# Kernel tuning notes

Measured on AMD Instinct MI355X. Metric: run time of the kernel, lower is better.

## Reference

```python
import jax, jax.numpy as jnp
import numpy as np

WIN_H, WIN_W = 4, 7
WIN = WIN_H * WIN_W  # 28 sample points == feature channels
GRID_OFF = (0.0, 40.0)
SPATIAL_SCALE = 1.0 / 0.4
BN_EPS = 1e-3


def setup_inputs() -> dict:
    key = jax.random.key(0)
    ks = jax.random.split(key, 5)
    B, Cin, H, W = 4, 256, 200, 176
    Cout, N = WIN, 2048
    x = jax.random.normal(ks[0], (B, Cin, H, W), dtype=jnp.float32)
    # boxes [x, y, z, w, l, h, r] in realistic KITTI ranges
    lo = jnp.array([0.0, -40.0, -3.0, 1.5, 3.2, 1.4, -np.pi], jnp.float32)
    hi = jnp.array([70.0, 40.0, 1.0, 2.0, 4.2, 1.8, np.pi], jnp.float32)
    u = jax.random.uniform(ks[1], (B, N, 7), dtype=jnp.float32)
    guided_anchors = lo + u * (hi - lo)
    w1 = jax.random.normal(ks[2], (Cout, Cin, 3, 3), jnp.float32) * 0.02
    gamma = jnp.ones((Cout,), jnp.float32)
    beta = jnp.zeros((Cout,), jnp.float32)
    running_mean = jnp.zeros((Cout,), jnp.float32)
    running_var = jnp.ones((Cout,), jnp.float32)
    w2 = jax.random.normal(ks[3], (Cout, Cout, 1, 1), jnp.float32) * 0.05
    return dict(x=x, guided_anchors=guided_anchors, w1=w1, gamma=gamma,
                beta=beta, running_mean=running_mean, running_var=running_var, w2=w2)


def _convs(x, w1, gamma, beta, mean, var, w2):
    dn = ('NCHW', 'OIHW', 'NCHW')
    y = jax.lax.conv_general_dilated(x, w1, (1, 1), 'SAME', dimension_numbers=dn)
    scale = gamma * jax.lax.rsqrt(var + BN_EPS)
    y = y * scale[:, None, None] + (beta - mean * scale)[:, None, None]  # BN (inference)
    y = jax.nn.relu(y)
    return jax.lax.conv_general_dilated(y, w2, (1, 1), 'SAME', dimension_numbers=dn)


def _gen_sample_grid(box5):
    xg, yg, wg, lg, rg = (box5[:, i] for i in range(5))
    c = jnp.cos(rg)[:, None, None]
    s = jnp.sin(rg)[:, None, None]
    xx = (jnp.linspace(-0.5, 0.5, WIN_H)[None, :] * wg[:, None])[:, :, None]  # (N,4,1)
    yy = (jnp.linspace(-0.5, 0.5, WIN_W)[None, :] * lg[:, None])[:, None, :]  # (N,1,7)
    xpix = xx * c + yy * s + xg[:, None, None]  # (N,4,7)
    ypix = yy * c - xx * s + yg[:, None, None]  # (N,4,7)
    xs = ((jnp.transpose(xpix, (1, 2, 0)) + GRID_OFF[0]) * SPATIAL_SCALE).reshape(WIN, -1)
    ys = ((jnp.transpose(ypix, (1, 2, 0)) + GRID_OFF[1]) * SPATIAL_SCALE).reshape(WIN, -1)
    return xs, ys


def _bilinear_sample(img, xs, ys):
    # img: (C,H,W); xs, ys: (C,N) pixel coords (align_corners=True semantics,
    # zero padding outside) -> (C,N). Channel c samples at grid row c.
    C, H, W = img.shape
    x0 = jnp.floor(xs); y0 = jnp.floor(ys)
    wx = xs - x0; wy = ys - y0
    cidx = jnp.arange(C)[:, None]

    def gather(yf, xf):
        yi = yf.astype(jnp.int32); xi = xf.astype(jnp.int32)
        valid = (yf >= 0) & (yf <= H - 1) & (xf >= 0) & (xf <= W - 1)
        v = img[cidx, jnp.clip(yi, 0, H - 1), jnp.clip(xi, 0, W - 1)]
        return jnp.where(valid, v, 0.0)

    return (gather(y0, x0) * (1 - wx) * (1 - wy)
            + gather(y0, x0 + 1) * wx * (1 - wy)
            + gather(y0 + 1, x0) * (1 - wx) * wy
            + gather(y0 + 1, x0 + 1) * wx * wy)


def reference(x, guided_anchors, w1, gamma, beta, running_mean, running_var, w2):
    feat = _convs(x, w1, gamma, beta, running_mean, running_var, w2)  # (B,28,H,W)
    box5 = guided_anchors[:, :, jnp.array([0, 1, 3, 4, 6])]           # (B,N,5)
    xs, ys = jax.vmap(_gen_sample_grid)(box5)                          # (B,28,N) each
    vals = jax.vmap(_bilinear_sample)(feat, xs, ys)                    # (B,28,N)
    scores = jnp.mean(vals, axis=1)                                    # (B,N)
    return scores.reshape(-1)                                          # (B*N,)
```

## Files before the change

kernel.cpp:

```cpp
#include <hip/hip_runtime.h>
#include <hip/hip_bf16.h>

#define HH 200
#define WW 176
#define CIN 256
#define CO 28
#define BN_EPS 1e-3f

typedef __attribute__((ext_vector_type(8))) short short8;
typedef __attribute__((ext_vector_type(4))) float f32x4;

static __device__ __forceinline__ ushort f2bf(float f) {
    __hip_bfloat16 h = __float2bfloat16(f);
    return __builtin_bit_cast(ushort, h);
}

__global__ void prep_k(const float* __restrict__ w1, const float* __restrict__ gamma,
                       const float* __restrict__ beta, const float* __restrict__ mean,
                       const float* __restrict__ var, ushort* __restrict__ w1b,
                       float* __restrict__ shift)
{
    int idx = blockIdx.x * 256 + threadIdx.x;
    if (idx < CO) {
        float sc = gamma[idx] * rsqrtf(var[idx] + BN_EPS);
        shift[idx] = beta[idx] - mean[idx] * sc;
    }
    if (idx < 8 * 9 * 2 * 64 * 8) {
        int j   = idx & 7;
        int l   = (idx >> 3) & 63;
        int n   = (idx >> 9) & 1;
        int rem = idx >> 10;
        int t   = rem % 9;
        int h   = rem / 9;
        int co = n * 16 + (l & 15);
        int ci = h * 32 + (l >> 4) * 8 + j;
        float v = 0.f;
        if (co < CO) {
            float sc = gamma[co] * rsqrtf(var[co] + BN_EPS);
            v = w1[(co * CIN + ci) * 9 + t] * sc;
        }
        w1b[idx] = f2bf(v);
    }
}

__global__ __launch_bounds__(256, 3) void conv_mfma_k(
    const float* __restrict__ x, const ushort* __restrict__ w1b,
    const float* __restrict__ shift, float* __restrict__ y1)
{
    __shared__ uint4 sbuf[2][180 * 4];

    const int tid  = threadIdx.x;
    const int lane = tid & 63;
    const int w    = tid >> 6;

    const int NB = 11 * 25 * 4;
    const int q = NB / 8, r = NB % 8;
    const int bid  = blockIdx.x;
    const int xcd  = bid & 7;
    const int rank = bid >> 3;
    const int tile = (xcd < r ? xcd * (q + 1) : r * (q + 1) + (xcd - r) * q) + rank;

    const int tx  = tile % 11;
    const int rem = tile / 11;
    const int ty  = rem % 25;
    const int b   = rem / 25;
    const int x0  = tx * 16, y0 = ty * 8;

    const float* xb = x + (size_t)b * CIN * HH * WW;

    int  soff[3]; bool sval[3]; bool sp[3];
#pragma unroll
    for (int it = 0; it < 3; ++it) {
        int p = it * 64 + lane;
        sp[it] = p < 180;
        int rr = p / 18, cc = p - rr * 18;
        int gy = y0 + rr - 1, gx = x0 + cc - 1;
        bool v = (gy >= 0) & (gy < HH) & (gx >= 0) & (gx < WW) & sp[it];
        sval[it] = v;
        soff[it] = v ? gy * WW + gx : 0;
    }

    float pre[3][8];

    auto issue_x = [&](int h) {
        const float* pl = xb + (size_t)(h * 32 + w * 8) * (HH * WW);
#pragma unroll
        for (int it = 0; it < 3; ++it) {
            if (sp[it]) {
#pragma unroll
                for (int j = 0; j < 8; ++j)
                    pre[it][j] = pl[(size_t)j * (HH * WW) + soff[it]];
            }
        }
    };

    auto wr_x = [&](int bi) {
#pragma unroll
        for (int it = 0; it < 3; ++it) {
            if (sp[it]) {
                int p = it * 64 + lane;
                ushort u[8];
#pragma unroll
                for (int j = 0; j < 8; ++j)
                    u[j] = sval[it] ? f2bf(pre[it][j]) : (ushort)0;
                uint4 val;
                val.x = (uint)u[0] | ((uint)u[1] << 16);
                val.y = (uint)u[2] | ((uint)u[3] << 16);
                val.z = (uint)u[4] | ((uint)u[5] << 16);
                val.w = (uint)u[6] | ((uint)u[7] << 16);
                sbuf[bi][p * 4 + ((w + p) & 3)] = val;
            }
        }
    };

    f32x4 acc[2][2];
#pragma unroll
    for (int m = 0; m < 2; ++m)
#pragma unroll
        for (int n = 0; n < 2; ++n)
            acc[m][n] = (f32x4){0.f, 0.f, 0.f, 0.f};

    issue_x(0);
    wr_x(0);
    __syncthreads();

#pragma unroll 1
    for (int h = 0; h < 8; ++h) {
        short8 wreg[9][2];
        {
            const ushort* wsrc = w1b + (size_t)h * 9216;
#pragma unroll
            for (int t = 0; t < 9; ++t)
#pragma unroll
                for (int n = 0; n < 2; ++n)
                    wreg[t][n] = *(const short8*)(wsrc + (size_t)((t * 2 + n) * 64 + lane) * 8);
        }
        if (h < 7) issue_x(h + 1);
        __builtin_amdgcn_sched_barrier(0);

        {
            const uint4* sb = sbuf[h & 1];
            short8 av[4][3];
#pragma unroll
            for (int rr = 0; rr < 4; ++rr) {
#pragma unroll
                for (int dx = 0; dx < 3; ++dx) {
                    int p = (2 * w + rr) * 18 + (lane & 15) + dx;
                    av[rr][dx] = __builtin_bit_cast(short8, sb[p * 4 + (((lane >> 4) + p) & 3)]);
                }
            }
#pragma unroll
            for (int t = 0; t < 9; ++t) {
                const int dy = t / 3, dx = t % 3;
#pragma unroll
                for (int m = 0; m < 2; ++m) {
                    short8 af = av[m + dy][dx];
                    acc[m][0] = __builtin_amdgcn_mfma_f32_16x16x32_bf16(af, wreg[t][0], acc[m][0], 0, 0, 0);
                    acc[m][1] = __builtin_amdgcn_mfma_f32_16x16x32_bf16(af, wreg[t][1], acc[m][1], 0, 0, 0);
                }
            }
        }
        __builtin_amdgcn_sched_barrier(0);

        if (h < 7) {
            wr_x((h + 1) & 1);
            __syncthreads();
        }
    }

    const int co0 = lane & 15;
    const int co1 = 16 + co0;
    const float s0 = shift[co0];
    const float s1 = (co1 < CO) ? shift[co1] : 0.f;
#pragma unroll
    for (int m = 0; m < 2; ++m) {
        int gy = y0 + 2 * w + m;
#pragma unroll
        for (int reg = 0; reg < 4; ++reg) {
            int gx = x0 + (lane >> 4) * 4 + reg;
            float* yp = y1 + ((size_t)(b * HH + gy) * WW + gx) * CO;
            float v0 = acc[m][0][reg] + s0;
            yp[co0] = v0 > 0.f ? v0 : 0.f;
            if (co1 < CO) {
                float v1 = acc[m][1][reg] + s1;
                yp[co1] = v1 > 0.f ? v1 : 0.f;
            }
        }
    }
}

__global__ __launch_bounds__(224) void sample_k(
    const float* __restrict__ y1, const float* __restrict__ ga,
    const float* __restrict__ w2, float* __restrict__ out)
{
    __shared__ float red[224];
    const int lb  = threadIdx.x / CO;
    const int k   = threadIdx.x % CO;
    const int box = blockIdx.x * 8 + lb;
    const int b   = box >> 11;

    const float* ap = ga + (size_t)box * 7;
    float xg = ap[0], yg = ap[1], wg = ap[3], lg = ap[4], rg = ap[6];
    float c = cosf(rg), s = sinf(rg);

    const int i = k / 7, j = k % 7;
    float xx = ((float)i * (1.f / 3.f) - 0.5f) * wg;
    float yy = ((float)j * (1.f / 6.f) - 0.5f) * lg;
    float xs = (xx * c + yy * s + xg) * 2.5f;
    float ys = (yy * c - xx * s + yg + 40.f) * 2.5f;

    float x0 = floorf(xs), y0 = floorf(ys);
    float wx = xs - x0,    wy = ys - y0;

    float w2r[CO];
    const float* w2p = w2 + k * CO;
#pragma unroll
    for (int q = 0; q < 7; ++q) {
        float4 t = ((const float4*)w2p)[q];
        w2r[4*q] = t.x; w2r[4*q+1] = t.y; w2r[4*q+2] = t.z; w2r[4*q+3] = t.w;
    }

    float val = 0.f;
    const float* yb = y1 + (size_t)b * HH * WW * CO;
#pragma unroll
    for (int cor = 0; cor < 4; ++cor) {
        float yf = y0 + (float)(cor >> 1);
        float xf = x0 + (float)(cor & 1);
        float cw = ((cor & 1) ? wx : 1.f - wx) * ((cor >> 1) ? wy : 1.f - wy);
        if (yf >= 0.f && yf <= (float)(HH - 1) && xf >= 0.f && xf <= (float)(WW - 1)) {
            int yi = (int)yf, xi = (int)xf;
            const float* p = yb + ((size_t)yi * WW + xi) * CO;
            float d = 0.f;
#pragma unroll
            for (int q = 0; q < 7; ++q) {
                float4 t = ((const float4*)p)[q];
                d = fmaf(w2r[4*q],   t.x, d);
                d = fmaf(w2r[4*q+1], t.y, d);
                d = fmaf(w2r[4*q+2], t.z, d);
                d = fmaf(w2r[4*q+3], t.w, d);
            }
            val = fmaf(cw, d, val);
        }
    }

    red[threadIdx.x] = val;
    __syncthreads();
    if (k == 0) {
        float sum = 0.f;
#pragma unroll
        for (int q = 0; q < CO; ++q) sum += red[lb * CO + q];
        out[box] = sum * (1.f / 28.f);
    }
}

extern "C" void kernel_launch(void* const* d_in, const int* in_sizes, int n_in,
                              void* d_out, int out_size, void* d_ws, size_t ws_size,
                              hipStream_t stream) {
    const float* x     = (const float*)d_in[0];
    const float* ga    = (const float*)d_in[1];
    const float* w1    = (const float*)d_in[2];
    const float* gamma = (const float*)d_in[3];
    const float* beta  = (const float*)d_in[4];
    const float* mean  = (const float*)d_in[5];
    const float* var   = (const float*)d_in[6];
    const float* w2    = (const float*)d_in[7];
    float* out = (float*)d_out;

    ushort* w1b   = (ushort*)d_ws;
    float*  shift = (float*)((char*)d_ws + 147456);
    float*  y1    = (float*)((char*)d_ws + 147968);

    prep_k<<<(8 * 9 * 2 * 64 * 8 + 255) / 256, 256, 0, stream>>>(
        w1, gamma, beta, mean, var, w1b, shift);

    conv_mfma_k<<<11 * 25 * 4, 256, 0, stream>>>(x, w1b, shift, y1);

    sample_k<<<(4 * 2048) / 8, 224, 0, stream>>>(y1, ga, w2, out);
}
```

Baseline: 86.49 us.

## Pre-transpose input to padded NHWC bf16 and drop LDS staging in conv

Adds two kernels: one zeroes the borders of a padded buffer, the other converts the NCHW fp32 input into a spatially padded NHWC bf16 layout. The conv kernel then reads A fragments straight from global memory as 16-byte vectors, with no LDS double-buffering, no barriers and no per-iteration bounds checks, and loads weights per tap instead of holding them all in registers. Occupancy is raised to 4 waves per SIMD. The cost is an extra full pass that reads x and writes a roughly 74 MB intermediate, and the conv now relies on cache for the 3x3 reuse rather than on LDS.

```diff
diff --git a/kernel.cpp b/kernel.cpp
--- a/kernel.cpp
+++ b/kernel.cpp
@@ -5,6 +5,8 @@
 #define WW 176
 #define CIN 256
 #define CO 28
+#define XH 202
+#define XW 178
 #define BN_EPS 1e-3f
 
 typedef __attribute__((ext_vector_type(8))) short short8;
@@ -43,12 +45,61 @@
     }
 }
 
-__global__ __launch_bounds__(256, 3) void conv_mfma_k(
-    const float* __restrict__ x, const ushort* __restrict__ w1b,
+__global__ __launch_bounds__(256) void pad_k(ushort* __restrict__ xtp)
+{
+    const int row = blockIdx.x;
+    const int y   = row % XH;
+    uint4* base = (uint4*)(xtp + (size_t)row * XW * 256);
+    const uint4 z = {0u, 0u, 0u, 0u};
+    if (y == 0 || y == XH - 1) {
+        for (int i = threadIdx.x; i < XW * 32; i += 256) base[i] = z;
+    } else if (threadIdx.x < 64) {
+        int px = threadIdx.x >> 5;
+        int i  = threadIdx.x & 31;
+        base[(px ? (XW - 1) : 0) * 32 + i] = z;
+    }
+}
+
+__global__ __launch_bounds__(256) void xt_k(const float* __restrict__ x,
+                                            ushort* __restrict__ xtp)
+{
+    const int bid = blockIdx.x;
+    const int xc  = bid % 11;
+    const int rem = bid / 11;
+    const int y   = rem % HH;
+    const int b   = rem / HH;
+    const int px  = threadIdx.x & 15;
+    const int cig = threadIdx.x >> 4;
+    const int gx  = xc * 16 + px;
+
+    const float* xp = x + ((size_t)b * CIN + cig * 16) * (HH * WW) + y * WW + gx;
+    float v[16];
+#pragma unroll
+    for (int j = 0; j < 16; ++j) v[j] = xp[(size_t)j * (HH * WW)];
+
+    ushort u[16];
+#pragma unroll
+    for (int j = 0; j < 16; ++j) u[j] = f2bf(v[j]);
+
+    uint4 a, c;
+    a.x = (uint)u[0]  | ((uint)u[1]  << 16);
+    a.y = (uint)u[2]  | ((uint)u[3]  << 16);
+    a.z = (uint)u[4]  | ((uint)u[5]  << 16);
+    a.w = (uint)u[6]  | ((uint)u[7]  << 16);
+    c.x = (uint)u[8]  | ((uint)u[9]  << 16);
+    c.y = (uint)u[10] | ((uint)u[11] << 16);
+    c.z = (uint)u[12] | ((uint)u[13] << 16);
+    c.w = (uint)u[14] | ((uint)u[15] << 16);
+
+    ushort* dst = xtp + (((size_t)(b * XH + y + 1)) * XW + gx + 1) * 256 + cig * 16;
+    ((uint4*)dst)[0] = a;
+    ((uint4*)dst)[1] = c;
+}
+
+__global__ __launch_bounds__(256, 4) void conv_mfma_k(
+    const ushort* __restrict__ xtp, const ushort* __restrict__ w1b,
     const float* __restrict__ shift, float* __restrict__ y1)
 {
-    __shared__ uint4 sbuf[2][180 * 4];
-
     const int tid  = threadIdx.x;
     const int lane = tid & 63;
     const int w    = tid >> 6;
@@ -66,52 +117,11 @@
     const int b   = rem / 25;
     const int x0  = tx * 16, y0 = ty * 8;
 
-    const float* xb = x + (size_t)b * CIN * HH * WW;
-
-    int  soff[3]; bool sval[3]; bool sp[3];
-#pragma unroll
-    for (int it = 0; it < 3; ++it) {
-        int p = it * 64 + lane;
-        sp[it] = p < 180;
-        int rr = p / 18, cc = p - rr * 18;
-        int gy = y0 + rr - 1, gx = x0 + cc - 1;
-        bool v = (gy >= 0) & (gy < HH) & (gx >= 0) & (gx < WW) & sp[it];
-        sval[it] = v;
-        soff[it] = v ? gy * WW + gx : 0;
-    }
-
-    float pre[3][8];
-
-    auto issue_x = [&](int h) {
-        const float* pl = xb + (size_t)(h * 32 + w * 8) * (HH * WW);
-#pragma unroll
-        for (int it = 0; it < 3; ++it) {
-            if (sp[it]) {
-#pragma unroll
-                for (int j = 0; j < 8; ++j)
-                    pre[it][j] = pl[(size_t)j * (HH * WW) + soff[it]];
-            }
-        }
-    };
-
-    auto wr_x = [&](int bi) {
-#pragma unroll
-        for (int it = 0; it < 3; ++it) {
-            if (sp[it]) {
-                int p = it * 64 + lane;
-                ushort u[8];
-#pragma unroll
-                for (int j = 0; j < 8; ++j)
-                    u[j] = sval[it] ? f2bf(pre[it][j]) : (ushort)0;
-                uint4 val;
-                val.x = (uint)u[0] | ((uint)u[1] << 16);
-                val.y = (uint)u[2] | ((uint)u[3] << 16);
-                val.z = (uint)u[4] | ((uint)u[5] << 16);
-                val.w = (uint)u[6] | ((uint)u[7] << 16);
-                sbuf[bi][p * 4 + ((w + p) & 3)] = val;
-            }
-        }
-    };
+    const int c_  = lane & 15;
+    const int oct = lane >> 4;
+
+    const ushort* abase = xtp
+        + (((size_t)(b * XH + y0 + 2 * w) * XW) + x0 + c_) * 256 + oct * 8;
 
     f32x4 acc[2][2];
 #pragma unroll
@@ -120,56 +130,33 @@
         for (int n = 0; n < 2; ++n)
             acc[m][n] = (f32x4){0.f, 0.f, 0.f, 0.f};
 
-    issue_x(0);
-    wr_x(0);
-    __syncthreads();
-
 #pragma unroll 1
     for (int h = 0; h < 8; ++h) {
-        short8 wreg[9][2];
-        {
-            const ushort* wsrc = w1b + (size_t)h * 9216;
-#pragma unroll
-            for (int t = 0; t < 9; ++t)
-#pragma unroll
-                for (int n = 0; n < 2; ++n)
-                    wreg[t][n] = *(const short8*)(wsrc + (size_t)((t * 2 + n) * 64 + lane) * 8);
-        }
-        if (h < 7) issue_x(h + 1);
-        __builtin_amdgcn_sched_barrier(0);
-
-        {
-            const uint4* sb = sbuf[h & 1];
-            short8 av[4][3];
-#pragma unroll
-            for (int rr = 0; rr < 4; ++rr) {
-#pragma unroll
-                for (int dx = 0; dx < 3; ++dx) {
-                    int p = (2 * w + rr) * 18 + (lane & 15) + dx;
-                    av[rr][dx] = __builtin_bit_cast(short8, sb[p * 4 + (((lane >> 4) + p) & 3)]);
-                }
+        const ushort* ab = abase + h * 32;
+        short8 av[4][3];
+#pragma unroll
+        for (int rl = 0; rl < 4; ++rl)
+#pragma unroll
+            for (int dx = 0; dx < 3; ++dx)
+                av[rl][dx] = *(const short8*)(ab + ((size_t)rl * XW + dx) * 256);
+
+        const ushort* wsrc = w1b + (size_t)h * 9216 + lane * 8;
+#pragma unroll
+        for (int t = 0; t < 9; ++t) {
+            const int dy = t / 3, dx = t % 3;
+            short8 b0 = *(const short8*)(wsrc + (size_t)(t * 2 + 0) * 512);
+            short8 b1 = *(const short8*)(wsrc + (size_t)(t * 2 + 1) * 512);
+#pragma unroll
+            for (int m = 0; m < 2; ++m) {
+                short8 af = av[m + dy][dx];
+                acc[m][0] = __builtin_amdgcn_mfma_f32_16x16x32_bf16(af, b0, acc[m][0], 0, 0, 0);
+                acc[m][1] = __builtin_amdgcn_mfma_f32_16x16x32_bf16(af, b1, acc[m][1], 0, 0, 0);
             }
-#pragma unroll
-            for (int t = 0; t < 9; ++t) {
-                const int dy = t / 3, dx = t % 3;
-#pragma unroll
-                for (int m = 0; m < 2; ++m) {
-                    short8 af = av[m + dy][dx];
-                    acc[m][0] = __builtin_amdgcn_mfma_f32_16x16x32_bf16(af, wreg[t][0], acc[m][0], 0, 0, 0);
-                    acc[m][1] = __builtin_amdgcn_mfma_f32_16x16x32_bf16(af, wreg[t][1], acc[m][1], 0, 0, 0);
-                }
-            }
-        }
-        __builtin_amdgcn_sched_barrier(0);
-
-        if (h < 7) {
-            wr_x((h + 1) & 1);
-            __syncthreads();
-        }
-    }
-
-    const int co0 = lane & 15;
-    const int co1 = 16 + co0;
+        }
+    }
+
+    const int co0 = c_;
+    const int co1 = 16 + c_;
     const float s0 = shift[co0];
     const float s1 = (co1 < CO) ? shift[co1] : 0.f;
 #pragma unroll
@@ -177,7 +164,7 @@
         int gy = y0 + 2 * w + m;
 #pragma unroll
         for (int reg = 0; reg < 4; ++reg) {
-            int gx = x0 + (lane >> 4) * 4 + reg;
+            int gx = x0 + oct * 4 + reg;
             float* yp = y1 + ((size_t)(b * HH + gy) * WW + gx) * CO;
             float v0 = acc[m][0][reg] + s0;
             yp[co0] = v0 > 0.f ? v0 : 0.f;
@@ -268,12 +255,16 @@
 
     ushort* w1b   = (ushort*)d_ws;
     float*  shift = (float*)((char*)d_ws + 147456);
-    float*  y1    = (float*)((char*)d_ws + 147968);
+    ushort* xtp   = (ushort*)((char*)d_ws + 147968);
+    float*  y1    = (float*)((char*)d_ws + 147968 + 73637888);
 
     prep_k<<<(8 * 9 * 2 * 64 * 8 + 255) / 256, 256, 0, stream>>>(
         w1, gamma, beta, mean, var, w1b, shift);
 
-    conv_mfma_k<<<11 * 25 * 4, 256, 0, stream>>>(x, w1b, shift, y1);
+    pad_k<<<4 * XH, 256, 0, stream>>>(xtp);
+    xt_k<<<4 * HH * 11, 256, 0, stream>>>(x, xtp);
+
+    conv_mfma_k<<<11 * 25 * 4, 256, 0, stream>>>(xtp, w1b, shift, y1);
 
     sample_k<<<(4 * 2048) / 8, 224, 0, stream>>>(y1, ga, w2, out);
 }
```

Result: slower. 160.2 us (+85.2%).

## Deepen input prefetch to two stages and stream conv weights per tap

Applied to the files above, without the earlier changes.

The 3x3 conv loop is fully unrolled and uses two register buffers for the input tile. Global loads for step h+2 are in flight while step h computes and step h+1's data is written to LDS. Weights are no longer loaded as all 18 fragments up front; they stream through a 3-slot rotating buffer, two taps ahead of the MFMAs. The aim is to hide global-memory latency for the input planes while keeping register pressure in check, but the extra prefetch registers and full unrolling could lower occupancy or grow code size.

```diff
diff --git a/kernel.cpp b/kernel.cpp
--- a/kernel.cpp
+++ b/kernel.cpp
@@ -80,38 +80,7 @@
         soff[it] = v ? gy * WW + gx : 0;
     }
 
-    float pre[3][8];
-
-    auto issue_x = [&](int h) {
-        const float* pl = xb + (size_t)(h * 32 + w * 8) * (HH * WW);
-#pragma unroll
-        for (int it = 0; it < 3; ++it) {
-            if (sp[it]) {
-#pragma unroll
-                for (int j = 0; j < 8; ++j)
-                    pre[it][j] = pl[(size_t)j * (HH * WW) + soff[it]];
-            }
-        }
-    };
-
-    auto wr_x = [&](int bi) {
-#pragma unroll
-        for (int it = 0; it < 3; ++it) {
-            if (sp[it]) {
-                int p = it * 64 + lane;
-                ushort u[8];
-#pragma unroll
-                for (int j = 0; j < 8; ++j)
-                    u[j] = sval[it] ? f2bf(pre[it][j]) : (ushort)0;
-                uint4 val;
-                val.x = (uint)u[0] | ((uint)u[1] << 16);
-                val.y = (uint)u[2] | ((uint)u[3] << 16);
-                val.z = (uint)u[4] | ((uint)u[5] << 16);
-                val.w = (uint)u[6] | ((uint)u[7] << 16);
-                sbuf[bi][p * 4 + ((w + p) & 3)] = val;
-            }
-        }
-    };
+    float pre0[3][8], pre1[3][8];
 
     f32x4 acc[2][2];
 #pragma unroll
@@ -120,53 +89,103 @@
         for (int n = 0; n < 2; ++n)
             acc[m][n] = (f32x4){0.f, 0.f, 0.f, 0.f};
 
-    issue_x(0);
-    wr_x(0);
+#define ISSUE_X(h, PRE)                                                     \
+    {                                                                       \
+        const float* pl = xb + (size_t)((h) * 32 + w * 8) * (HH * WW);      \
+        _Pragma("unroll")                                                   \
+        for (int it = 0; it < 3; ++it) {                                    \
+            if (sp[it]) {                                                   \
+                _Pragma("unroll")                                           \
+                for (int j = 0; j < 8; ++j)                                 \
+                    PRE[it][j] = pl[(size_t)j * (HH * WW) + soff[it]];      \
+            }                                                               \
+        }                                                                   \
+    }
+
+#define WR_X(PRE, BI)                                                       \
+    {                                                                       \
+        _Pragma("unroll")                                                   \
+        for (int it = 0; it < 3; ++it) {                                    \
+            if (sp[it]) {                                                   \
+                int p = it * 64 + lane;                                     \
+                ushort u[8];                                                \
+                _Pragma("unroll")                                           \
+                for (int j = 0; j < 8; ++j)                                 \
+                    u[j] = sval[it] ? f2bf(PRE[it][j]) : (ushort)0;         \
+                uint4 val;                                                  \
+                val.x = (uint)u[0] | ((uint)u[1] << 16);                    \
+                val.y = (uint)u[2] | ((uint)u[3] << 16);                    \
+                val.z = (uint)u[4] | ((uint)u[5] << 16);                    \
+                val.w = (uint)u[6] | ((uint)u[7] << 16);                    \
+                sbuf[BI][p * 4 + ((w + p) & 3)] = val;                      \
+            }                                                               \
+        }                                                                   \
+    }
+
+#define COMPUTE(h)                                                          \
+    {                                                                       \
+        const uint4* sb = sbuf[(h) & 1];                                    \
+        short8 av[4][3];                                                    \
+        _Pragma("unroll")                                                   \
+        for (int rl = 0; rl < 4; ++rl) {                                    \
+            _Pragma("unroll")                                               \
+            for (int dx = 0; dx < 3; ++dx) {                                \
+                int p = (2 * w + rl) * 18 + (lane & 15) + dx;               \
+                av[rl][dx] = __builtin_bit_cast(short8,                     \
+                    sb[p * 4 + (((lane >> 4) + p) & 3)]);                   \
+            }                                                               \
+        }                                                                   \
+        const ushort* wsrc = w1b + (size_t)(h) * 9216 + lane * 8;           \
+        short8 wq[3][2];                                                    \
+        _Pragma("unroll")                                                   \
+        for (int n = 0; n < 2; ++n) {                                       \
+            wq[0][n] = *(const short8*)(wsrc + (size_t)(0 * 2 + n) * 512);  \
+            wq[1][n] = *(const short8*)(wsrc + (size_t)(1 * 2 + n) * 512);  \
+        }                                                                   \
+        _Pragma("unroll")                                                   \
+        for (int t = 0; t < 9; ++t) {                                       \
+            if (t + 2 < 9) {                                                \
+                _Pragma("unroll")                                           \
+                for (int n = 0; n < 2; ++n)                                 \
+                    wq[(t + 2) % 3][n] =                                    \
+                        *(const short8*)(wsrc + (size_t)((t + 2) * 2 + n) * 512); \
+            }                                                               \
+            const int dy = t / 3, dx = t % 3;                               \
+            _Pragma("unroll")                                               \
+            for (int m = 0; m < 2; ++m) {                                   \
+                short8 af = av[m + dy][dx];                                 \
+                acc[m][0] = __builtin_amdgcn_mfma_f32_16x16x32_bf16(        \
+                    af, wq[t % 3][0], acc[m][0], 0, 0, 0);                  \
+                acc[m][1] = __builtin_amdgcn_mfma_f32_16x16x32_bf16(        \
+                    af, wq[t % 3][1], acc[m][1], 0, 0, 0);                  \
+            }                                                               \
+        }                                                                   \
+    }
+
+#define STEP(h, PREI, PREW)                                                 \
+    {                                                                       \
+        if ((h) + 2 < 8) ISSUE_X((h) + 2, PREI);                            \
+        __builtin_amdgcn_sched_barrier(0);                                  \
+        COMPUTE(h);                                                         \
+        if ((h) < 7) {                                                      \
+            WR_X(PREW, ((h) + 1) & 1);                                      \
+            __syncthreads();                                                \
+        }                                                                   \
+    }
+
+    ISSUE_X(0, pre0);
+    ISSUE_X(1, pre1);
+    WR_X(pre0, 0);
     __syncthreads();
 
-#pragma unroll 1
-    for (int h = 0; h < 8; ++h) {
-        short8 wreg[9][2];
-        {
-            const ushort* wsrc = w1b + (size_t)h * 9216;
-#pragma unroll
-            for (int t = 0; t < 9; ++t)
-#pragma unroll
-                for (int n = 0; n < 2; ++n)
-                    wreg[t][n] = *(const short8*)(wsrc + (size_t)((t * 2 + n) * 64 + lane) * 8);
-        }
-        if (h < 7) issue_x(h + 1);
-        __builtin_amdgcn_sched_barrier(0);
-
-        {
-            const uint4* sb = sbuf[h & 1];
-            short8 av[4][3];
-#pragma unroll
-            for (int rr = 0; rr < 4; ++rr) {
-#pragma unroll
-                for (int dx = 0; dx < 3; ++dx) {
-                    int p = (2 * w + rr) * 18 + (lane & 15) + dx;
-                    av[rr][dx] = __builtin_bit_cast(short8, sb[p * 4 + (((lane >> 4) + p) & 3)]);
-                }
-            }
-#pragma unroll
-            for (int t = 0; t < 9; ++t) {
-                const int dy = t / 3, dx = t % 3;
-#pragma unroll
-                for (int m = 0; m < 2; ++m) {
-                    short8 af = av[m + dy][dx];
-                    acc[m][0] = __builtin_amdgcn_mfma_f32_16x16x32_bf16(af, wreg[t][0], acc[m][0], 0, 0, 0);
-                    acc[m][1] = __builtin_amdgcn_mfma_f32_16x16x32_bf16(af, wreg[t][1], acc[m][1], 0, 0, 0);
-                }
-            }
-        }
-        __builtin_amdgcn_sched_barrier(0);
-
-        if (h < 7) {
-            wr_x((h + 1) & 1);
-            __syncthreads();
-        }
-    }
+    STEP(0, pre0, pre1);
+    STEP(1, pre1, pre0);
+    STEP(2, pre0, pre1);
+    STEP(3, pre1, pre0);
+    STEP(4, pre0, pre1);
+    STEP(5, pre1, pre0);
+    STEP(6, pre0, pre1);
+    STEP(7, pre1, pre0);
 
     const int co0 = lane & 15;
     const int co1 = 16 + co0;
```

New measurement: 84.19 us. 2.7% less time.

## Hand-schedule conv pipeline with inline-asm loads and explicit vmcnt waits

Applied to the files above, without the earlier changes.

Rewrites the conv main loop as a fully unrolled, hand-pipelined sequence. Global loads for x and the weights are issued through inline asm with scalar base plus vector offset, and s_waitcnt counts are placed by hand so the next slice's x loads overlap the current MFMA work. Weights are now loaded after the LDS pack step instead of at the top of each iteration. The LDS buffer is padded to 192 positions so the p<180 guard can be dropped, and the swizzle changes to (p>>1) to alter bank mapping. The hand-written waitcnt logic is fragile, and the extra padded lanes issue loads at offset 0.

```diff
diff --git a/kernel.cpp b/kernel.cpp
--- a/kernel.cpp
+++ b/kernel.cpp
@@ -47,11 +47,14 @@
     const float* __restrict__ x, const ushort* __restrict__ w1b,
     const float* __restrict__ shift, float* __restrict__ y1)
 {
-    __shared__ uint4 sbuf[2][180 * 4];
+    __shared__ uint4 sbuf[2][192 * 4];
 
     const int tid  = threadIdx.x;
     const int lane = tid & 63;
     const int w    = tid >> 6;
+    const int wu   = __builtin_amdgcn_readfirstlane(w);
+    const int c_   = lane & 15;
+    const int oct  = lane >> 4;
 
     const int NB = 11 * 25 * 4;
     const int q = NB / 8, r = NB % 8;
@@ -68,50 +71,23 @@
 
     const float* xb = x + (size_t)b * CIN * HH * WW;
 
-    int  soff[3]; bool sval[3]; bool sp[3];
+    int  soff[3]; bool sval[3];
 #pragma unroll
     for (int it = 0; it < 3; ++it) {
         int p = it * 64 + lane;
-        sp[it] = p < 180;
         int rr = p / 18, cc = p - rr * 18;
         int gy = y0 + rr - 1, gx = x0 + cc - 1;
-        bool v = (gy >= 0) & (gy < HH) & (gx >= 0) & (gx < WW) & sp[it];
+        bool v = (gy >= 0) & (gy < HH) & (gx >= 0) & (gx < WW);
         sval[it] = v;
         soff[it] = v ? gy * WW + gx : 0;
     }
-
-    float pre[3][8];
-
-    auto issue_x = [&](int h) {
-        const float* pl = xb + (size_t)(h * 32 + w * 8) * (HH * WW);
-#pragma unroll
-        for (int it = 0; it < 3; ++it) {
-            if (sp[it]) {
-#pragma unroll
-                for (int j = 0; j < 8; ++j)
-                    pre[it][j] = pl[(size_t)j * (HH * WW) + soff[it]];
-            }
-        }
-    };
-
-    auto wr_x = [&](int bi) {
-#pragma unroll
-        for (int it = 0; it < 3; ++it) {
-            if (sp[it]) {
-                int p = it * 64 + lane;
-                ushort u[8];
-#pragma unroll
-                for (int j = 0; j < 8; ++j)
-                    u[j] = sval[it] ? f2bf(pre[it][j]) : (ushort)0;
-                uint4 val;
-                val.x = (uint)u[0] | ((uint)u[1] << 16);
-                val.y = (uint)u[2] | ((uint)u[3] << 16);
-                val.z = (uint)u[4] | ((uint)u[5] << 16);
-                val.w = (uint)u[6] | ((uint)u[7] << 16);
-                sbuf[bi][p * 4 + ((w + p) & 3)] = val;
-            }
-        }
-    };
+    const uint voff0 = (uint)(soff[0] * 4);
+    const uint voff1 = (uint)(soff[1] * 4);
+    const uint voff2 = (uint)(soff[2] * 4);
+    const uint wvoff = (uint)(lane * 16);
+
+    float  xr[24];
+    short8 wr[18];
 
     f32x4 acc[2][2];
 #pragma unroll
@@ -120,56 +96,123 @@
         for (int n = 0; n < 2; ++n)
             acc[m][n] = (f32x4){0.f, 0.f, 0.f, 0.f};
 
-    issue_x(0);
-    wr_x(0);
-    __syncthreads();
-
-#pragma unroll 1
-    for (int h = 0; h < 8; ++h) {
-        short8 wreg[9][2];
-        {
-            const ushort* wsrc = w1b + (size_t)h * 9216;
-#pragma unroll
-            for (int t = 0; t < 9; ++t)
-#pragma unroll
-                for (int n = 0; n < 2; ++n)
-                    wreg[t][n] = *(const short8*)(wsrc + (size_t)((t * 2 + n) * 64 + lane) * 8);
-        }
-        if (h < 7) issue_x(h + 1);
-        __builtin_amdgcn_sched_barrier(0);
-
-        {
-            const uint4* sb = sbuf[h & 1];
-            short8 av[4][3];
-#pragma unroll
-            for (int rr = 0; rr < 4; ++rr) {
-#pragma unroll
-                for (int dx = 0; dx < 3; ++dx) {
-                    int p = (2 * w + rr) * 18 + (lane & 15) + dx;
-                    av[rr][dx] = __builtin_bit_cast(short8, sb[p * 4 + (((lane >> 4) + p) & 3)]);
-                }
-            }
-#pragma unroll
-            for (int t = 0; t < 9; ++t) {
-                const int dy = t / 3, dx = t % 3;
-#pragma unroll
-                for (int m = 0; m < 2; ++m) {
-                    short8 af = av[m + dy][dx];
-                    acc[m][0] = __builtin_amdgcn_mfma_f32_16x16x32_bf16(af, wreg[t][0], acc[m][0], 0, 0, 0);
-                    acc[m][1] = __builtin_amdgcn_mfma_f32_16x16x32_bf16(af, wreg[t][1], acc[m][1], 0, 0, 0);
-                }
-            }
-        }
-        __builtin_amdgcn_sched_barrier(0);
-
-        if (h < 7) {
-            wr_x((h + 1) & 1);
-            __syncthreads();
-        }
-    }
-
-    const int co0 = lane & 15;
-    const int co1 = 16 + co0;
+#define XLOAD(h)                                                              \
+    {                                                                         \
+        _Pragma("unroll")                                                     \
+        for (int j = 0; j < 8; ++j) {                                         \
+            const float* bj = xb + (size_t)((h) * 32 + wu * 8 + j) * 35200;   \
+            asm volatile("global_load_dword %0, %1, %2"                       \
+                         : "=v"(xr[0 + j]) : "v"(voff0), "s"(bj));            \
+            asm volatile("global_load_dword %0, %1, %2"                       \
+                         : "=v"(xr[8 + j]) : "v"(voff1), "s"(bj));            \
+            asm volatile("global_load_dword %0, %1, %2"                       \
+                         : "=v"(xr[16 + j]) : "v"(voff2), "s"(bj));           \
+        }                                                                     \
+    }
+
+#define WLOAD(h)                                                              \
+    {                                                                         \
+        _Pragma("unroll")                                                     \
+        for (int k = 0; k < 18; ++k) {                                        \
+            const ushort* bk = w1b + (size_t)(h) * 9216 + k * 512;            \
+            asm volatile("global_load_dwordx4 %0, %1, %2"                     \
+                         : "=v"(wr[k]) : "v"(wvoff), "s"(bk));                \
+        }                                                                     \
+    }
+
+#define WAITW(N)                                                              \
+    asm volatile("s_waitcnt vmcnt(" #N ")"                                    \
+        : "+v"(wr[0]), "+v"(wr[1]), "+v"(wr[2]), "+v"(wr[3]), "+v"(wr[4]),    \
+          "+v"(wr[5]), "+v"(wr[6]), "+v"(wr[7]), "+v"(wr[8]));                \
+    asm volatile("s_waitcnt vmcnt(" #N ")"                                    \
+        : "+v"(wr[9]), "+v"(wr[10]), "+v"(wr[11]), "+v"(wr[12]),              \
+          "+v"(wr[13]), "+v"(wr[14]), "+v"(wr[15]), "+v"(wr[16]),             \
+          "+v"(wr[17]));                                                      \
+    __builtin_amdgcn_sched_barrier(0);
+
+#define WAITX()                                                               \
+    asm volatile("s_waitcnt vmcnt(0)"                                         \
+        : "+v"(xr[0]), "+v"(xr[1]), "+v"(xr[2]), "+v"(xr[3]), "+v"(xr[4]),    \
+          "+v"(xr[5]), "+v"(xr[6]), "+v"(xr[7]), "+v"(xr[8]), "+v"(xr[9]),    \
+          "+v"(xr[10]), "+v"(xr[11]));                                        \
+    asm volatile("s_waitcnt vmcnt(0)"                                         \
+        : "+v"(xr[12]), "+v"(xr[13]), "+v"(xr[14]), "+v"(xr[15]),             \
+          "+v"(xr[16]), "+v"(xr[17]), "+v"(xr[18]), "+v"(xr[19]),             \
+          "+v"(xr[20]), "+v"(xr[21]), "+v"(xr[22]), "+v"(xr[23]));            \
+    __builtin_amdgcn_sched_barrier(0);
+
+#define PACK_WR(BI)                                                           \
+    {                                                                         \
+        _Pragma("unroll")                                                     \
+        for (int it = 0; it < 3; ++it) {                                      \
+            int p = it * 64 + lane;                                           \
+            ushort u[8];                                                      \
+            _Pragma("unroll")                                                 \
+            for (int j = 0; j < 8; ++j)                                       \
+                u[j] = sval[it] ? f2bf(xr[it * 8 + j]) : (ushort)0;           \
+            uint4 val;                                                        \
+            val.x = (uint)u[0] | ((uint)u[1] << 16);                          \
+            val.y = (uint)u[2] | ((uint)u[3] << 16);                          \
+            val.z = (uint)u[4] | ((uint)u[5] << 16);                          \
+            val.w = (uint)u[6] | ((uint)u[7] << 16);                          \
+            sbuf[BI][p * 4 + ((w + (p >> 1)) & 3)] = val;                     \
+        }                                                                     \
+    }
+
+#define COMPUTE(h)                                                            \
+    {                                                                         \
+        const uint4* sb = sbuf[(h) & 1];                                      \
+        _Pragma("unroll")                                                     \
+        for (int dx = 0; dx < 3; ++dx) {                                      \
+            short8 av[4];                                                     \
+            _Pragma("unroll")                                                 \
+            for (int rl = 0; rl < 4; ++rl) {                                  \
+                int p = (2 * w + rl) * 18 + c_ + dx;                          \
+                av[rl] = __builtin_bit_cast(short8,                           \
+                    sb[p * 4 + ((oct + (p >> 1)) & 3)]);                      \
+            }                                                                 \
+            _Pragma("unroll")                                                 \
+            for (int dy = 0; dy < 3; ++dy) {                                  \
+                const int t = dy * 3 + dx;                                    \
+                _Pragma("unroll")                                             \
+                for (int m = 0; m < 2; ++m) {                                 \
+                    acc[m][0] = __builtin_amdgcn_mfma_f32_16x16x32_bf16(      \
+                        av[m + dy], wr[t * 2 + 0], acc[m][0], 0, 0, 0);       \
+                    acc[m][1] = __builtin_amdgcn_mfma_f32_16x16x32_bf16(      \
+                        av[m + dy], wr[t * 2 + 1], acc[m][1], 0, 0, 0);       \
+                }                                                             \
+            }                                                                 \
+        }                                                                     \
+    }
+
+#define BODY(h)                                                               \
+    {                                                                         \
+        XLOAD((h) + 1);                                                       \
+        WAITW(24)                                                             \
+        COMPUTE(h);                                                           \
+        WAITX()                                                               \
+        PACK_WR(((h) + 1) & 1);                                               \
+        WLOAD((h) + 1);                                                       \
+        asm volatile("s_waitcnt lgkmcnt(0)");                                 \
+        __builtin_amdgcn_sched_barrier(0);                                    \
+        __builtin_amdgcn_s_barrier();                                         \
+    }
+
+    WLOAD(0);
+    XLOAD(0);
+    WAITW(0)
+    WAITX()
+    PACK_WR(0);
+    asm volatile("s_waitcnt lgkmcnt(0)");
+    __builtin_amdgcn_sched_barrier(0);
+    __builtin_amdgcn_s_barrier();
+
+    BODY(0) BODY(1) BODY(2) BODY(3) BODY(4) BODY(5) BODY(6)
+    WAITW(0)
+    COMPUTE(7);
+
+    const int co0 = c_;
+    const int co1 = 16 + c_;
     const float s0 = shift[co0];
     const float s1 = (co1 < CO) ? shift[co1] : 0.f;
 #pragma unroll
@@ -177,7 +220,7 @@
         int gy = y0 + 2 * w + m;
 #pragma unroll
         for (int reg = 0; reg < 4; ++reg) {
-            int gx = x0 + (lane >> 4) * 4 + reg;
+            int gx = x0 + oct * 4 + reg;
             float* yp = y1 + ((size_t)(b * HH + gy) * WW + gx) * CO;
             float v0 = acc[m][0][reg] + s0;
             yp[co0] = v0 > 0.f ? v0 : 0.f;
```

Result: faster. 83.46 us (-3.5%).
